# Optimization experiments

Measured on AMD Instinct MI355X. Metric: run time of the kernel, lower is better.

The kernel has to match this reference:

```python
import jax, jax.numpy as jnp
import numpy as np

N = 50000      # num nodes
E = 800000     # edges per hypergraph (avg degree 16)
G = 3          # hyper_edge_num
D_IN = 128
D_OUT = 128


def setup_inputs() -> dict:
    key = jax.random.key(0)
    ks = jax.random.split(key, 6)
    company_emb = jax.random.normal(ks[0], (N, D_IN), dtype=jnp.float32)
    # nn.Linear weight [out, in], glorot-ish scaling
    W = jax.random.normal(ks[1], (D_OUT, D_IN), dtype=jnp.float32) / np.sqrt(D_IN).astype(np.float32)
    alpha = jax.random.normal(ks[2], (G, 1), dtype=jnp.float32)
    edge_rows = jax.random.randint(ks[3], (G, E), 0, N, dtype=jnp.int32)
    edge_cols = jax.random.randint(ks[4], (G, E), 0, N, dtype=jnp.int32)
    edge_vals = jax.random.normal(ks[5], (G, E), dtype=jnp.float32)
    return {
        "company_emb": company_emb,
        "W": W,
        "alpha": alpha,
        "edge_rows": edge_rows,
        "edge_cols": edge_cols,
        "edge_vals": edge_vals,
    }


def reference(company_emb, W, alpha, edge_rows, edge_cols, edge_vals):
    # shared dense projection: h = X @ W^T, [N, D_OUT]
    h = company_emb @ W.T

    def spmm(rows, cols, vals):
        # sparse Laplacian (COO) @ h : gather source rows, scale, scatter-add to dest rows
        msg = vals[:, None] * h[cols]                     # [E, D_OUT]
        return jax.ops.segment_sum(msg, rows, num_segments=N)

    aggs = jax.vmap(spmm)(edge_rows, edge_cols, edge_vals)  # [G, N, D_OUT]
    gate = jax.nn.sigmoid(alpha[:, 0])                       # [G]
    # res = sum_g sigmoid(alpha_g) * (L_g @ h)
    return jnp.einsum('g,gnd->nd', gate, aggs)
```

## Files before the change

kernel.cpp:

```cpp
#include <hip/hip_runtime.h>
#include <math.h>

#define NNODES 50000
#define NEDGE  800000
#define NG     3
#define D      128
#define GE     (NG*NEDGE)
#define NBUK   782
#define CH     4096
#define NBLK   ((GE + CH - 1) / CH)
#define OS     (NBUK + 1)
#define CAP2   3456

__device__ __forceinline__ unsigned short f2bf(float f) {
    unsigned u = __float_as_uint(f);
    return (unsigned short)((u + 0x7fffu + ((u >> 16) & 1u)) >> 16);
}

__global__ __launch_bounds__(256) void k_gemm(const float* __restrict__ X,
                                              const float* __restrict__ W,
                                              unsigned* __restrict__ hbits) {
    __shared__ float Xs[128 * 64];
    __shared__ float Ws[128 * 64];
    const int tid  = threadIdx.x;
    const int row0 = blockIdx.x * 64;
    const int col0 = blockIdx.y * 64;

    const int rl = tid & 63;
    const int kc = tid >> 6;
    int xr = row0 + rl; if (xr >= NNODES) xr = NNODES - 1;
    const float4* Xg = (const float4*)(X + (size_t)xr * D);
    const float4* Wg = (const float4*)(W + (size_t)(col0 + rl) * D);
#pragma unroll
    for (int it = 0; it < 8; ++it) {
        const int k4 = kc * 32 + it * 4;
        float4 xv = Xg[k4 >> 2];
        float4 wv = Wg[k4 >> 2];
        Xs[(k4 + 0) * 64 + rl] = xv.x;
        Xs[(k4 + 1) * 64 + rl] = xv.y;
        Xs[(k4 + 2) * 64 + rl] = xv.z;
        Xs[(k4 + 3) * 64 + rl] = xv.w;
        Ws[(k4 + 0) * 64 + rl] = wv.x;
        Ws[(k4 + 1) * 64 + rl] = wv.y;
        Ws[(k4 + 2) * 64 + rl] = wv.z;
        Ws[(k4 + 3) * 64 + rl] = wv.w;
    }
    __syncthreads();

    const int tx = tid & 15;
    const int ty = tid >> 4;
    float acc[4][4] = {};
    for (int k = 0; k < 128; ++k) {
        float4 xv4 = *(const float4*)&Xs[k * 64 + (ty << 2)];
        float4 wv4 = *(const float4*)&Ws[k * 64 + (tx << 2)];
        float xa[4] = {xv4.x, xv4.y, xv4.z, xv4.w};
        float wa[4] = {wv4.x, wv4.y, wv4.z, wv4.w};
#pragma unroll
        for (int i = 0; i < 4; ++i)
#pragma unroll
            for (int j = 0; j < 4; ++j)
                acc[i][j] += xa[i] * wa[j];
    }

#pragma unroll
    for (int i = 0; i < 4; ++i) {
        const int r = row0 + (ty << 2) + i;
        if (r < NNODES) {
            uint2 o;
            o.x = (unsigned)f2bf(acc[i][0]) | ((unsigned)f2bf(acc[i][1]) << 16);
            o.y = (unsigned)f2bf(acc[i][2]) | ((unsigned)f2bf(acc[i][3]) << 16);
            *(uint2*)&hbits[(size_t)r * 64 + ((col0 + (tx << 2)) >> 1)] = o;
        }
    }
}

__global__ __launch_bounds__(256) void k_bin(const int* __restrict__ rows,
                                             const int* __restrict__ cols,
                                             const float* __restrict__ vals,
                                             const float* __restrict__ alpha,
                                             uint2* __restrict__ out1,
                                             int* __restrict__ off1) {
    __shared__ uint2 stg[CH];
    __shared__ int sA[1024];
    __shared__ int sB[1024];
    __shared__ int lcur[NBUK];
    const int t   = threadIdx.x;
    const int blk = blockIdx.x;
    const int start = blk * CH;
    const int end   = (start + CH < GE) ? (start + CH) : GE;

    const float g0 = 1.0f / (1.0f + __expf(-alpha[0]));
    const float g1 = 1.0f / (1.0f + __expf(-alpha[1]));
    const float g2 = 1.0f / (1.0f + __expf(-alpha[2]));

    for (int i = t; i < 1024; i += 256) sA[i] = 0;
    __syncthreads();

    for (int idx = start + t, k = t; idx < end; idx += 256, k += 256) {
        const int r = rows[idx];
        const int c = cols[idx];
        const float v = vals[idx];
        const float gv = v * (idx < NEDGE ? g0 : (idx < 2 * NEDGE ? g1 : g2));
        uint2 rec;
        rec.x = ((unsigned)r << 16) | (unsigned)c;
        rec.y = __float_as_uint(gv);
        stg[k] = rec;
        atomicAdd(&sA[r >> 6], 1);
    }
    __syncthreads();

    int* src = sA; int* dst = sB;
    for (int off = 1; off < 1024; off <<= 1) {
        for (int i = t; i < 1024; i += 256)
            dst[i] = src[i] + ((i >= off) ? src[i - off] : 0);
        __syncthreads();
        int* tmp = src; src = dst; dst = tmp;
    }

    for (int b = t; b < NBUK; b += 256) {
        const int ex = b ? src[b - 1] : 0;
        lcur[b] = ex;
        off1[(size_t)blk * OS + b] = ex;
    }
    if (t == 0) off1[(size_t)blk * OS + NBUK] = src[NBUK - 1];
    __syncthreads();

    for (int idx = start + t, k = t; idx < end; idx += 256, k += 256) {
        const uint2 rec = stg[k];
        const int b = (int)(rec.x >> 22);
        const int pos = atomicAdd(&lcur[b], 1);
        out1[(size_t)blk * CH + pos] = rec;
    }
}

__global__ __launch_bounds__(512) void k_agg2(const unsigned* __restrict__ hbits,
                                              const uint2* __restrict__ out1,
                                              const int* __restrict__ off1,
                                              float* __restrict__ out) {
    __shared__ uint2 stg[CAP2];
    __shared__ unsigned short order[CAP2];
    __shared__ int sA[512];
    __shared__ int sB[512];
    __shared__ int rh[64], rbase[64], rcur[64];
    const int t = threadIdx.x;
    const int b = blockIdx.x;

    if (t < 64) rh[t] = 0;

    int s0 = 0, e0 = 0, s1 = 0, e1 = 0;
    s0 = off1[(size_t)t * OS + b];
    e0 = off1[(size_t)t * OS + b + 1];
    int myLen = e0 - s0;
    if (t + 512 < NBLK) {
        s1 = off1[(size_t)(t + 512) * OS + b];
        e1 = off1[(size_t)(t + 512) * OS + b + 1];
        myLen += e1 - s1;
    }
    sA[t] = myLen;
    __syncthreads();

    int* src = sA; int* dst = sB;
    for (int off = 1; off < 512; off <<= 1) {
        dst[t] = src[t] + ((t >= off) ? src[t - off] : 0);
        __syncthreads();
        int* tmp = src; src = dst; dst = tmp;
    }
    const int base = src[t] - myLen;

    int p = base;
    {
        const uint2* seg = out1 + (size_t)t * CH;
        for (int i = s0; i < e0; ++i, ++p) {
            if (p < CAP2) {
                const uint2 rec = seg[i];
                stg[p] = rec;
                atomicAdd(&rh[(rec.x >> 16) & 63u], 1);
            }
        }
        if (t + 512 < NBLK) {
            const uint2* seg2 = out1 + (size_t)(t + 512) * CH;
            for (int i = s1; i < e1; ++i, ++p) {
                if (p < CAP2) {
                    const uint2 rec = seg2[i];
                    stg[p] = rec;
                    atomicAdd(&rh[(rec.x >> 16) & 63u], 1);
                }
            }
        }
    }
    __syncthreads();

    if (t < 64) sA[t] = rh[t];
    __syncthreads();
    for (int off = 1; off < 64; off <<= 1) {
        int v = 0;
        if (t < 64) v = sA[t] + ((t >= off) ? sA[t - off] : 0);
        __syncthreads();
        if (t < 64) sA[t] = v;
        __syncthreads();
    }
    if (t < 64) { rbase[t] = sA[t] - rh[t]; rcur[t] = sA[t] - rh[t]; }
    __syncthreads();

    {
        const int lim = (base + myLen < CAP2) ? (base + myLen) : CAP2;
        for (int k = base; k < lim; ++k) {
            const int lr = (int)((stg[k].x >> 16) & 63u);
            const int pos = atomicAdd(&rcur[lr], 1);
            order[pos] = (unsigned short)k;
        }
    }
    __syncthreads();

    const int w    = t >> 6;
    const int lane = t & 63;
    for (int k = 0; k < 8; ++k) {
        const int lr  = (w << 3) + k;
        const int row = (b << 6) + lr;
        const int s   = rbase[lr];
        const int cnt = rh[lr];
        float2 acc = make_float2(0.f, 0.f);
        int i = 0;
        for (; i + 8 <= cnt; i += 8) {
            int idx8[8];
#pragma unroll
            for (int j = 0; j < 8; ++j) idx8[j] = order[s + i + j];
            uint2 m[8];
#pragma unroll
            for (int j = 0; j < 8; ++j) m[j] = stg[idx8[j]];
            unsigned hb[8];
#pragma unroll
            for (int j = 0; j < 8; ++j)
                hb[j] = hbits[(size_t)(m[j].x & 0xffffu) * 64 + lane];
#pragma unroll
            for (int j = 0; j < 8; ++j) {
                const float v = __uint_as_float(m[j].y);
                acc.x += v * __uint_as_float(hb[j] << 16);
                acc.y += v * __uint_as_float(hb[j] & 0xffff0000u);
            }
        }
        for (; i < cnt; ++i) {
            const uint2 m = stg[order[s + i]];
            const unsigned hbv = hbits[(size_t)(m.x & 0xffffu) * 64 + lane];
            const float v = __uint_as_float(m.y);
            acc.x += v * __uint_as_float(hbv << 16);
            acc.y += v * __uint_as_float(hbv & 0xffff0000u);
        }
        if (row < NNODES)
            ((float2*)out)[(size_t)row * 64 + lane] = acc;
    }
}

extern "C" void kernel_launch(void* const* d_in, const int* in_sizes, int n_in,
                              void* d_out, int out_size, void* d_ws, size_t ws_size,
                              hipStream_t stream) {
    const float* X     = (const float*)d_in[0];
    const float* W     = (const float*)d_in[1];
    const float* alpha = (const float*)d_in[2];
    const int*   rows  = (const int*)d_in[3];
    const int*   cols  = (const int*)d_in[4];
    const float* vals  = (const float*)d_in[5];
    float* out = (float*)d_out;

    char* ws = (char*)d_ws;
    unsigned* hbits = (unsigned*)(ws + 0);
    uint2*    out1  = (uint2*)  (ws + 12800000);
    int*      off1  = (int*)    (ws + 32002048);

    hipLaunchKernelGGL(k_gemm, dim3((NNODES + 63) / 64, 2), dim3(256), 0, stream, X, W, hbits);
    hipLaunchKernelGGL(k_bin, dim3(NBLK), dim3(256), 0, stream,
                       rows, cols, vals, alpha, out1, off1);
    hipLaunchKernelGGL(k_agg2, dim3(NBUK), dim3(512), 0, stream,
                       hbits, out1, off1, out);
}
```

Before: 258.7 us.

## Sort edges by column range and sync waves to improve gather cache locality

The aggregation kernel now buckets each row's edges into four source-column ranges and processes all rows range by range, with a block barrier between ranges. The goal is to keep the gathered h rows of concurrently running blocks within a smaller window so they stay in L2. The binning kernel drops its LDS staging buffer and instead reads the edge arrays twice, once to count and once to scatter. The scans are also made in-place, removing the double buffers. These changes add extra barriers and global re-reads, and they rely on columns being spread across the node range.

```diff
diff --git a/kernel.cpp b/kernel.cpp
--- a/kernel.cpp
+++ b/kernel.cpp
@@ -15,6 +15,10 @@
 __device__ __forceinline__ unsigned short f2bf(float f) {
     unsigned u = __float_as_uint(f);
     return (unsigned short)((u + 0x7fffu + ((u >> 16) & 1u)) >> 16);
+}
+
+__device__ __forceinline__ int col_range(int c) {
+    return (c >= 12500) + (c >= 25000) + (c >= 37500);
 }
 
 __global__ __launch_bounds__(256) void k_gemm(const float* __restrict__ X,
@@ -80,9 +84,7 @@
                                              const float* __restrict__ alpha,
                                              uint2* __restrict__ out1,
                                              int* __restrict__ off1) {
-    __shared__ uint2 stg[CH];
     __shared__ int sA[1024];
-    __shared__ int sB[1024];
     __shared__ int lcur[NBUK];
     const int t   = threadIdx.x;
     const int blk = blockIdx.x;
@@ -93,43 +95,45 @@
     const float g1 = 1.0f / (1.0f + __expf(-alpha[1]));
     const float g2 = 1.0f / (1.0f + __expf(-alpha[2]));
 
-    for (int i = t; i < 1024; i += 256) sA[i] = 0;
-    __syncthreads();
-
-    for (int idx = start + t, k = t; idx < end; idx += 256, k += 256) {
+#pragma unroll
+    for (int j = 0; j < 4; ++j) sA[t + j * 256] = 0;
+    __syncthreads();
+
+    for (int idx = start + t; idx < end; idx += 256)
+        atomicAdd(&sA[rows[idx] >> 6], 1);
+    __syncthreads();
+
+    for (int off = 1; off < 1024; off <<= 1) {
+        int v[4];
+#pragma unroll
+        for (int j = 0; j < 4; ++j) {
+            const int i = t + j * 256;
+            v[j] = sA[i] + ((i >= off) ? sA[i - off] : 0);
+        }
+        __syncthreads();
+#pragma unroll
+        for (int j = 0; j < 4; ++j) sA[t + j * 256] = v[j];
+        __syncthreads();
+    }
+
+    for (int b = t; b < NBUK; b += 256) {
+        const int ex = b ? sA[b - 1] : 0;
+        lcur[b] = ex;
+        off1[(size_t)blk * OS + b] = ex;
+    }
+    if (t == 0) off1[(size_t)blk * OS + NBUK] = sA[NBUK - 1];
+    __syncthreads();
+
+    for (int idx = start + t; idx < end; idx += 256) {
         const int r = rows[idx];
         const int c = cols[idx];
         const float v = vals[idx];
         const float gv = v * (idx < NEDGE ? g0 : (idx < 2 * NEDGE ? g1 : g2));
-        uint2 rec;
-        rec.x = ((unsigned)r << 16) | (unsigned)c;
-        rec.y = __float_as_uint(gv);
-        stg[k] = rec;
-        atomicAdd(&sA[r >> 6], 1);
-    }
-    __syncthreads();
-
-    int* src = sA; int* dst = sB;
-    for (int off = 1; off < 1024; off <<= 1) {
-        for (int i = t; i < 1024; i += 256)
-            dst[i] = src[i] + ((i >= off) ? src[i - off] : 0);
-        __syncthreads();
-        int* tmp = src; src = dst; dst = tmp;
-    }
-
-    for (int b = t; b < NBUK; b += 256) {
-        const int ex = b ? src[b - 1] : 0;
-        lcur[b] = ex;
-        off1[(size_t)blk * OS + b] = ex;
-    }
-    if (t == 0) off1[(size_t)blk * OS + NBUK] = src[NBUK - 1];
-    __syncthreads();
-
-    for (int idx = start + t, k = t; idx < end; idx += 256, k += 256) {
-        const uint2 rec = stg[k];
-        const int b = (int)(rec.x >> 22);
-        const int pos = atomicAdd(&lcur[b], 1);
-        out1[(size_t)blk * CH + pos] = rec;
+        const int pos = atomicAdd(&lcur[r >> 6], 1);
+        uint2 m;
+        m.x = ((unsigned)r << 16) | (unsigned)c;
+        m.y = __float_as_uint(gv);
+        out1[(size_t)blk * CH + pos] = m;
     }
 }
 
@@ -140,16 +144,17 @@
     __shared__ uint2 stg[CAP2];
     __shared__ unsigned short order[CAP2];
     __shared__ int sA[512];
-    __shared__ int sB[512];
-    __shared__ int rh[64], rbase[64], rcur[64];
+    __shared__ int rh2[256];
+    __shared__ int rb2[256];
+    __shared__ int rc2[256];
     const int t = threadIdx.x;
     const int b = blockIdx.x;
 
-    if (t < 64) rh[t] = 0;
-
-    int s0 = 0, e0 = 0, s1 = 0, e1 = 0;
-    s0 = off1[(size_t)t * OS + b];
-    e0 = off1[(size_t)t * OS + b + 1];
+    if (t < 256) rh2[t] = 0;
+
+    const int s0 = off1[(size_t)t * OS + b];
+    const int e0 = off1[(size_t)t * OS + b + 1];
+    int s1 = 0, e1 = 0;
     int myLen = e0 - s0;
     if (t + 512 < NBLK) {
         s1 = off1[(size_t)(t + 512) * OS + b];
@@ -159,22 +164,23 @@
     sA[t] = myLen;
     __syncthreads();
 
-    int* src = sA; int* dst = sB;
     for (int off = 1; off < 512; off <<= 1) {
-        dst[t] = src[t] + ((t >= off) ? src[t - off] : 0);
-        __syncthreads();
-        int* tmp = src; src = dst; dst = tmp;
-    }
-    const int base = src[t] - myLen;
-
-    int p = base;
+        const int v = sA[t] + ((t >= off) ? sA[t - off] : 0);
+        __syncthreads();
+        sA[t] = v;
+        __syncthreads();
+    }
+    const int base = sA[t] - myLen;
+
     {
+        int p = base;
         const uint2* seg = out1 + (size_t)t * CH;
         for (int i = s0; i < e0; ++i, ++p) {
             if (p < CAP2) {
                 const uint2 rec = seg[i];
                 stg[p] = rec;
-                atomicAdd(&rh[(rec.x >> 16) & 63u], 1);
+                const int key = (int)((rec.x >> 16) & 63u) * 4 + col_range((int)(rec.x & 0xffffu));
+                atomicAdd(&rh2[key], 1);
             }
         }
         if (t + 512 < NBLK) {
@@ -183,30 +189,32 @@
                 if (p < CAP2) {
                     const uint2 rec = seg2[i];
                     stg[p] = rec;
-                    atomicAdd(&rh[(rec.x >> 16) & 63u], 1);
+                    const int key = (int)((rec.x >> 16) & 63u) * 4 + col_range((int)(rec.x & 0xffffu));
+                    atomicAdd(&rh2[key], 1);
                 }
             }
         }
     }
     __syncthreads();
 
-    if (t < 64) sA[t] = rh[t];
-    __syncthreads();
-    for (int off = 1; off < 64; off <<= 1) {
+    if (t < 256) sA[t] = rh2[t];
+    __syncthreads();
+    for (int off = 1; off < 256; off <<= 1) {
         int v = 0;
-        if (t < 64) v = sA[t] + ((t >= off) ? sA[t - off] : 0);
-        __syncthreads();
-        if (t < 64) sA[t] = v;
-        __syncthreads();
-    }
-    if (t < 64) { rbase[t] = sA[t] - rh[t]; rcur[t] = sA[t] - rh[t]; }
+        if (t < 256) v = sA[t] + ((t >= off) ? sA[t - off] : 0);
+        __syncthreads();
+        if (t < 256) sA[t] = v;
+        __syncthreads();
+    }
+    if (t < 256) { rb2[t] = sA[t] - rh2[t]; rc2[t] = sA[t] - rh2[t]; }
     __syncthreads();
 
     {
         const int lim = (base + myLen < CAP2) ? (base + myLen) : CAP2;
         for (int k = base; k < lim; ++k) {
-            const int lr = (int)((stg[k].x >> 16) & 63u);
-            const int pos = atomicAdd(&rcur[lr], 1);
+            const uint2 rec = stg[k];
+            const int key = (int)((rec.x >> 16) & 63u) * 4 + col_range((int)(rec.x & 0xffffu));
+            const int pos = atomicAdd(&rc2[key], 1);
             order[pos] = (unsigned short)k;
         }
     }
@@ -214,40 +222,54 @@
 
     const int w    = t >> 6;
     const int lane = t & 63;
+    float2 acc[8];
+#pragma unroll
+    for (int k = 0; k < 8; ++k) acc[k] = make_float2(0.f, 0.f);
+
+    for (int rg = 0; rg < 4; ++rg) {
+#pragma unroll
+        for (int k = 0; k < 8; ++k) {
+            const int lr  = (w << 3) + k;
+            const int key = lr * 4 + rg;
+            const int s   = rb2[key];
+            const int cnt = rh2[key];
+            float2 a = acc[k];
+            int i = 0;
+            for (; i + 8 <= cnt; i += 8) {
+                int idx8[8];
+#pragma unroll
+                for (int j = 0; j < 8; ++j) idx8[j] = order[s + i + j];
+                uint2 m[8];
+#pragma unroll
+                for (int j = 0; j < 8; ++j) m[j] = stg[idx8[j]];
+                unsigned hb[8];
+#pragma unroll
+                for (int j = 0; j < 8; ++j)
+                    hb[j] = hbits[(size_t)(m[j].x & 0xffffu) * 64 + lane];
+#pragma unroll
+                for (int j = 0; j < 8; ++j) {
+                    const float v = __uint_as_float(m[j].y);
+                    a.x += v * __uint_as_float(hb[j] << 16);
+                    a.y += v * __uint_as_float(hb[j] & 0xffff0000u);
+                }
+            }
+            for (; i < cnt; ++i) {
+                const uint2 m = stg[order[s + i]];
+                const unsigned hbv = hbits[(size_t)(m.x & 0xffffu) * 64 + lane];
+                const float v = __uint_as_float(m.y);
+                a.x += v * __uint_as_float(hbv << 16);
+                a.y += v * __uint_as_float(hbv & 0xffff0000u);
+            }
+            acc[k] = a;
+        }
+        if (rg < 3) __syncthreads();
+    }
+
+#pragma unroll
     for (int k = 0; k < 8; ++k) {
-        const int lr  = (w << 3) + k;
-        const int row = (b << 6) + lr;
-        const int s   = rbase[lr];
-        const int cnt = rh[lr];
-        float2 acc = make_float2(0.f, 0.f);
-        int i = 0;
-        for (; i + 8 <= cnt; i += 8) {
-            int idx8[8];
-#pragma unroll
-            for (int j = 0; j < 8; ++j) idx8[j] = order[s + i + j];
-            uint2 m[8];
-#pragma unroll
-            for (int j = 0; j < 8; ++j) m[j] = stg[idx8[j]];
-            unsigned hb[8];
-#pragma unroll
-            for (int j = 0; j < 8; ++j)
-                hb[j] = hbits[(size_t)(m[j].x & 0xffffu) * 64 + lane];
-#pragma unroll
-            for (int j = 0; j < 8; ++j) {
-                const float v = __uint_as_float(m[j].y);
-                acc.x += v * __uint_as_float(hb[j] << 16);
-                acc.y += v * __uint_as_float(hb[j] & 0xffff0000u);
-            }
-        }
-        for (; i < cnt; ++i) {
-            const uint2 m = stg[order[s + i]];
-            const unsigned hbv = hbits[(size_t)(m.x & 0xffffu) * 64 + lane];
-            const float v = __uint_as_float(m.y);
-            acc.x += v * __uint_as_float(hbv << 16);
-            acc.y += v * __uint_as_float(hbv & 0xffff0000u);
-        }
+        const int row = (b << 6) + (w << 3) + k;
         if (row < NNODES)
-            ((float2*)out)[(size_t)row * 64 + lane] = acc;
+            ((float2*)out)[(size_t)row * 64 + lane] = acc[k];
     }
 }
 
```

New measurement: 293.2 us. 1.13x slower.

## Use bf16 MFMA for projection GEMM and precompute ranks in binning

Applied to the files above, without the earlier changes.

Replaces the FP32 SIMT shared-memory GEMM with a bf16 MFMA 16x16x32 kernel. A small prep kernel pre-swizzles W into MFMA fragment layout, and X is converted to bf16 in registers. The binning kernel now records each edge's intra-bucket rank from the counting atomic, which removes the second atomic pass and the double-buffered scan arrays. Rounding inputs to bf16 changes precision slightly, and one extra tiny kernel launch is added.

```diff
diff --git a/kernel.cpp b/kernel.cpp
--- a/kernel.cpp
+++ b/kernel.cpp
@@ -12,64 +12,76 @@
 #define OS     (NBUK + 1)
 #define CAP2   3456
 
+typedef __attribute__((ext_vector_type(8))) short bf16x8;
+typedef __attribute__((ext_vector_type(4))) float f32x4;
+
 __device__ __forceinline__ unsigned short f2bf(float f) {
     unsigned u = __float_as_uint(f);
     return (unsigned short)((u + 0x7fffu + ((u >> 16) & 1u)) >> 16);
 }
 
+__global__ void k_wprep(const float* __restrict__ W, uint4* __restrict__ Wf) {
+    const int t = threadIdx.x;
+    for (int i = t; i < 2048; i += 256) {
+        const int nt   = i >> 8;
+        const int kc   = (i >> 6) & 3;
+        const int lane = i & 63;
+        const int n  = nt * 16 + (lane & 15);
+        const int k0 = kc * 32 + (lane >> 4) * 8;
+        const float* src = W + (size_t)n * 128 + k0;
+        unsigned u0 = (unsigned)f2bf(src[0]) | ((unsigned)f2bf(src[1]) << 16);
+        unsigned u1 = (unsigned)f2bf(src[2]) | ((unsigned)f2bf(src[3]) << 16);
+        unsigned u2 = (unsigned)f2bf(src[4]) | ((unsigned)f2bf(src[5]) << 16);
+        unsigned u3 = (unsigned)f2bf(src[6]) | ((unsigned)f2bf(src[7]) << 16);
+        Wf[i] = make_uint4(u0, u1, u2, u3);
+    }
+}
+
 __global__ __launch_bounds__(256) void k_gemm(const float* __restrict__ X,
-                                              const float* __restrict__ W,
-                                              unsigned* __restrict__ hbits) {
-    __shared__ float Xs[128 * 64];
-    __shared__ float Ws[128 * 64];
-    const int tid  = threadIdx.x;
-    const int row0 = blockIdx.x * 64;
-    const int col0 = blockIdx.y * 64;
-
-    const int rl = tid & 63;
-    const int kc = tid >> 6;
-    int xr = row0 + rl; if (xr >= NNODES) xr = NNODES - 1;
-    const float4* Xg = (const float4*)(X + (size_t)xr * D);
-    const float4* Wg = (const float4*)(W + (size_t)(col0 + rl) * D);
-#pragma unroll
-    for (int it = 0; it < 8; ++it) {
-        const int k4 = kc * 32 + it * 4;
-        float4 xv = Xg[k4 >> 2];
-        float4 wv = Wg[k4 >> 2];
-        Xs[(k4 + 0) * 64 + rl] = xv.x;
-        Xs[(k4 + 1) * 64 + rl] = xv.y;
-        Xs[(k4 + 2) * 64 + rl] = xv.z;
-        Xs[(k4 + 3) * 64 + rl] = xv.w;
-        Ws[(k4 + 0) * 64 + rl] = wv.x;
-        Ws[(k4 + 1) * 64 + rl] = wv.y;
-        Ws[(k4 + 2) * 64 + rl] = wv.z;
-        Ws[(k4 + 3) * 64 + rl] = wv.w;
-    }
-    __syncthreads();
-
-    const int tx = tid & 15;
-    const int ty = tid >> 4;
-    float acc[4][4] = {};
-    for (int k = 0; k < 128; ++k) {
-        float4 xv4 = *(const float4*)&Xs[k * 64 + (ty << 2)];
-        float4 wv4 = *(const float4*)&Ws[k * 64 + (tx << 2)];
-        float xa[4] = {xv4.x, xv4.y, xv4.z, xv4.w};
-        float wa[4] = {wv4.x, wv4.y, wv4.z, wv4.w};
-#pragma unroll
-        for (int i = 0; i < 4; ++i)
-#pragma unroll
-            for (int j = 0; j < 4; ++j)
-                acc[i][j] += xa[i] * wa[j];
-    }
-
-#pragma unroll
-    for (int i = 0; i < 4; ++i) {
-        const int r = row0 + (ty << 2) + i;
-        if (r < NNODES) {
-            uint2 o;
-            o.x = (unsigned)f2bf(acc[i][0]) | ((unsigned)f2bf(acc[i][1]) << 16);
-            o.y = (unsigned)f2bf(acc[i][2]) | ((unsigned)f2bf(acc[i][3]) << 16);
-            *(uint2*)&hbits[(size_t)r * 64 + ((col0 + (tx << 2)) >> 1)] = o;
+                                              const uint4* __restrict__ Wf,
+                                              unsigned short* __restrict__ hb16) {
+    __shared__ uint4 Wl[2048];
+    const int t = threadIdx.x;
+#pragma unroll
+    for (int j = 0; j < 8; ++j) Wl[t + j * 256] = Wf[t + j * 256];
+    __syncthreads();
+
+    const int w    = t >> 6;
+    const int lane = t & 63;
+    const int q    = lane >> 4;
+    const int ml   = lane & 15;
+    const int m0   = blockIdx.x * 64 + w * 16;
+
+    int xr = m0 + ml; if (xr >= NNODES) xr = NNODES - 1;
+    const float* xrow = X + (size_t)xr * 128;
+
+    bf16x8 xf[4];
+#pragma unroll
+    for (int kc = 0; kc < 4; ++kc) {
+        const int k0 = kc * 32 + q * 8;
+        float4 a = *(const float4*)(xrow + k0);
+        float4 b = *(const float4*)(xrow + k0 + 4);
+        bf16x8 v;
+        v[0] = (short)f2bf(a.x); v[1] = (short)f2bf(a.y);
+        v[2] = (short)f2bf(a.z); v[3] = (short)f2bf(a.w);
+        v[4] = (short)f2bf(b.x); v[5] = (short)f2bf(b.y);
+        v[6] = (short)f2bf(b.z); v[7] = (short)f2bf(b.w);
+        xf[kc] = v;
+    }
+
+#pragma unroll
+    for (int nt = 0; nt < 8; ++nt) {
+        f32x4 acc = {0.f, 0.f, 0.f, 0.f};
+#pragma unroll
+        for (int kc = 0; kc < 4; ++kc) {
+            const bf16x8 wf = *(const bf16x8*)&Wl[(nt * 4 + kc) * 64 + lane];
+            acc = __builtin_amdgcn_mfma_f32_16x16x32_bf16(xf[kc], wf, acc, 0, 0, 0);
+        }
+#pragma unroll
+        for (int r = 0; r < 4; ++r) {
+            const int row = m0 + q * 4 + r;
+            if (row < NNODES)
+                hb16[(size_t)row * 128 + nt * 16 + ml] = f2bf(acc[r]);
         }
     }
 }
@@ -81,9 +93,8 @@
                                              uint2* __restrict__ out1,
                                              int* __restrict__ off1) {
     __shared__ uint2 stg[CH];
+    __shared__ unsigned short rnk[CH];
     __shared__ int sA[1024];
-    __shared__ int sB[1024];
-    __shared__ int lcur[NBUK];
     const int t   = threadIdx.x;
     const int blk = blockIdx.x;
     const int start = blk * CH;
@@ -93,7 +104,8 @@
     const float g1 = 1.0f / (1.0f + __expf(-alpha[1]));
     const float g2 = 1.0f / (1.0f + __expf(-alpha[2]));
 
-    for (int i = t; i < 1024; i += 256) sA[i] = 0;
+#pragma unroll
+    for (int j = 0; j < 4; ++j) sA[t + j * 256] = 0;
     __syncthreads();
 
     for (int idx = start + t, k = t; idx < end; idx += 256, k += 256) {
@@ -105,30 +117,31 @@
         rec.x = ((unsigned)r << 16) | (unsigned)c;
         rec.y = __float_as_uint(gv);
         stg[k] = rec;
-        atomicAdd(&sA[r >> 6], 1);
-    }
-    __syncthreads();
-
-    int* src = sA; int* dst = sB;
+        rnk[k] = (unsigned short)atomicAdd(&sA[r >> 6], 1);
+    }
+    __syncthreads();
+
     for (int off = 1; off < 1024; off <<= 1) {
-        for (int i = t; i < 1024; i += 256)
-            dst[i] = src[i] + ((i >= off) ? src[i - off] : 0);
-        __syncthreads();
-        int* tmp = src; src = dst; dst = tmp;
-    }
-
-    for (int b = t; b < NBUK; b += 256) {
-        const int ex = b ? src[b - 1] : 0;
-        lcur[b] = ex;
-        off1[(size_t)blk * OS + b] = ex;
-    }
-    if (t == 0) off1[(size_t)blk * OS + NBUK] = src[NBUK - 1];
-    __syncthreads();
+        int v[4];
+#pragma unroll
+        for (int j = 0; j < 4; ++j) {
+            const int i = t + j * 256;
+            v[j] = sA[i] + ((i >= off) ? sA[i - off] : 0);
+        }
+        __syncthreads();
+#pragma unroll
+        for (int j = 0; j < 4; ++j) sA[t + j * 256] = v[j];
+        __syncthreads();
+    }
+
+    for (int b = t; b < NBUK; b += 256)
+        off1[(size_t)blk * OS + b] = b ? sA[b - 1] : 0;
+    if (t == 0) off1[(size_t)blk * OS + NBUK] = sA[NBUK - 1];
 
     for (int idx = start + t, k = t; idx < end; idx += 256, k += 256) {
         const uint2 rec = stg[k];
         const int b = (int)(rec.x >> 22);
-        const int pos = atomicAdd(&lcur[b], 1);
+        const int pos = (b ? sA[b - 1] : 0) + (int)rnk[k];
         out1[(size_t)blk * CH + pos] = rec;
     }
 }
@@ -147,9 +160,9 @@
 
     if (t < 64) rh[t] = 0;
 
-    int s0 = 0, e0 = 0, s1 = 0, e1 = 0;
-    s0 = off1[(size_t)t * OS + b];
-    e0 = off1[(size_t)t * OS + b + 1];
+    const int s0 = off1[(size_t)t * OS + b];
+    const int e0 = off1[(size_t)t * OS + b + 1];
+    int s1 = 0, e1 = 0;
     int myLen = e0 - s0;
     if (t + 512 < NBLK) {
         s1 = off1[(size_t)(t + 512) * OS + b];
@@ -167,8 +180,8 @@
     }
     const int base = src[t] - myLen;
 
-    int p = base;
     {
+        int p = base;
         const uint2* seg = out1 + (size_t)t * CH;
         for (int i = s0; i < e0; ++i, ++p) {
             if (p < CAP2) {
@@ -263,11 +276,14 @@
     float* out = (float*)d_out;
 
     char* ws = (char*)d_ws;
-    unsigned* hbits = (unsigned*)(ws + 0);
-    uint2*    out1  = (uint2*)  (ws + 12800000);
-    int*      off1  = (int*)    (ws + 32002048);
-
-    hipLaunchKernelGGL(k_gemm, dim3((NNODES + 63) / 64, 2), dim3(256), 0, stream, X, W, hbits);
+    unsigned*       hbits = (unsigned*)(ws + 0);
+    unsigned short* hb16  = (unsigned short*)(ws + 0);
+    uint2*          out1  = (uint2*)(ws + 12800000);
+    int*            off1  = (int*)  (ws + 32002048);
+    uint4*          Wf    = (uint4*)(ws + 33837408);
+
+    hipLaunchKernelGGL(k_wprep, dim3(1), dim3(256), 0, stream, W, Wf);
+    hipLaunchKernelGGL(k_gemm, dim3(NBUK), dim3(256), 0, stream, X, Wf, hb16);
     hipLaunchKernelGGL(k_bin, dim3(NBLK), dim3(256), 0, stream,
                        rows, cols, vals, alpha, out1, off1);
     hipLaunchKernelGGL(k_agg2, dim3(NBUK), dim3(512), 0, stream,
```

Result: faster. 239.4 us (-7.5%).
